# Optimization experiments

Hardware: AMD Instinct MI355X
Metric: run time of the kernel (lower is better)

Reference implementation:

```python
import jax, jax.numpy as jnp
import numpy as np

R, IN, H, O = 4, 1024, 4, 1024
HID4 = H * O  # 4096, GATConv output after flatten(1)
N_PRE, N_HYP, N_COMB = 1024, 1024, 2048
E_PRE, E_HYP, E_COMB = 8192, 8192, 16384


def setup_inputs() -> dict:
    key = jax.random.key(0)
    ks = jax.random.split(key, 24)
    w = lambda i, shape: jax.random.normal(ks[i], shape, dtype=jnp.float32) * 0.02
    return {
        'x_pre': jax.random.normal(ks[0], (N_PRE, IN), dtype=jnp.float32),
        'x_hyp': jax.random.normal(ks[1], (N_HYP, IN), dtype=jnp.float32),
        'x_comb': jax.random.normal(ks[2], (N_COMB, IN), dtype=jnp.float32),
        'src_pre': jax.random.randint(ks[3], (R, E_PRE), 0, N_PRE, dtype=jnp.int32),
        'dst_pre': jax.random.randint(ks[4], (R, E_PRE), 0, N_PRE, dtype=jnp.int32),
        'src_hyp': jax.random.randint(ks[5], (R, E_HYP), 0, N_HYP, dtype=jnp.int32),
        'dst_hyp': jax.random.randint(ks[6], (R, E_HYP), 0, N_HYP, dtype=jnp.int32),
        'src_comb': jax.random.randint(ks[7], (R, E_COMB), 0, N_COMB, dtype=jnp.int32),
        'dst_comb': jax.random.randint(ks[8], (R, E_COMB), 0, N_COMB, dtype=jnp.int32),
        'W1': w(9, (R, IN, HID4)),
        'al1': w(10, (R, H, O)),
        'ar1': w(11, (R, H, O)),
        'b1': w(12, (R, HID4)),
        'res1': w(13, (R, IN, HID4)),
        'W2': w(14, (R, HID4, HID4)),
        'al2': w(15, (R, H, O)),
        'ar2': w(16, (R, H, O)),
        'b2': w(17, (R, HID4)),
        'Wp': w(18, (3 * HID4, 3 * 1024)),
        'bp': w(19, (3 * 1024,)),
        'Wc1': w(20, (3 * 1024, 1024)),
        'bc1': w(21, (1024,)),
        'Wc2': w(22, (1024, 3)),
        'bc2': w(23, (3,)),
    }


def _gat_rel(x, src, dst, W, al, ar, b, res, N, identity_res):
    # DGL GATConv (eval mode, dropout off): shared fc, edge softmax, residual, bias
    feat = (x @ W).reshape(N, H, O)                       # [N,H,O]
    el = (feat * al[None]).sum(-1)                        # [N,H]
    er = (feat * ar[None]).sum(-1)                        # [N,H]
    e = jax.nn.leaky_relu(el[src] + er[dst], 0.2)         # [E,H]
    m = jax.ops.segment_max(e, dst, num_segments=N)
    m = jnp.where(jnp.isfinite(m), m, 0.0)                # zero-in-degree safe
    p = jnp.exp(e - m[dst])
    s = jax.ops.segment_sum(p, dst, num_segments=N)
    alpha = p / jnp.where(s[dst] > 0, s[dst], 1.0)        # [E,H]
    out = jax.ops.segment_sum(alpha[:, :, None] * feat[src], dst, num_segments=N)
    resval = x.reshape(N, H, O) if identity_res else (x @ res).reshape(N, H, O)
    return out + resval + b.reshape(1, H, O)


def _hetero_conv(x, src_r, dst_r, W_r, al_r, ar_r, b_r, res_r, N):
    # HeteroGraphConv(aggregate='mean') over R relations, scan to bound memory
    acc0 = jnp.zeros((N, H, O), dtype=x.dtype)
    if res_r is None:
        def body(acc, rel):
            src, dst, W, al, ar, b = rel
            return acc + _gat_rel(x, src, dst, W, al, ar, b, None, N, True), None
        acc, _ = jax.lax.scan(body, acc0, (src_r, dst_r, W_r, al_r, ar_r, b_r))
    else:
        def body(acc, rel):
            src, dst, W, al, ar, b, res = rel
            return acc + _gat_rel(x, src, dst, W, al, ar, b, res, N, False), None
        acc, _ = jax.lax.scan(body, acc0, (src_r, dst_r, W_r, al_r, ar_r, b_r, res_r))
    return acc / R


def _rgat(x, src, dst, W1, al1, ar1, b1, res1, W2, al2, ar2, b2, N):
    h = _hetero_conv(x, src, dst, W1, al1, ar1, b1, res1, N)
    h = jax.nn.elu(h.reshape(N, HID4))                    # flatten(1) + ELU
    h = _hetero_conv(h, src, dst, W2, al2, ar2, b2, None, N)
    return h.reshape(N, HID4)


def reference(x_pre, x_hyp, x_comb, src_pre, dst_pre, src_hyp, dst_hyp,
              src_comb, dst_comb, W1, al1, ar1, b1, res1, W2, al2, ar2, b2,
              Wp, bp, Wc1, bc1, Wc2, bc2):
    rp = _rgat(x_pre, src_pre, dst_pre, W1, al1, ar1, b1, res1, W2, al2, ar2, b2, N_PRE).mean(0, keepdims=True)
    rh = _rgat(x_hyp, src_hyp, dst_hyp, W1, al1, ar1, b1, res1, W2, al2, ar2, b2, N_HYP).mean(0, keepdims=True)
    rc = _rgat(x_comb, src_comb, dst_comb, W1, al1, ar1, b1, res1, W2, al2, ar2, b2, N_COMB).mean(0, keepdims=True)
    z = jnp.concatenate([rp, rh, rc], axis=1) @ Wp + bp   # graph_repr_proj
    hcls = jax.nn.relu(z @ Wc1 + bc1)                     # classifier MLP (dropout off)
    return hcls @ Wc2 + bc2                               # logits [1, n_classes]
```

## Files before the change

kernel.cpp:

```cpp
#include <hip/hip_runtime.h>
#include <math.h>

#define HID 4096
#define NMAX 2048
#define EMAX 16384
#define RREL 4
#define NTOT 4096

typedef unsigned short ushortT;
typedef __attribute__((ext_vector_type(8))) short short8;
typedef __attribute__((ext_vector_type(4))) float floatx4;

#define GLDS(gp, lp)                                                                        \
  __builtin_amdgcn_global_load_lds((const __attribute__((address_space(1))) unsigned*)(gp), \
                                   (__attribute__((address_space(3))) unsigned*)(lp), 16, 0, 0)

__device__ __forceinline__ ushortT f2b(float f) {
  unsigned u = __float_as_uint(f);
  u = u + 0x7fffu + ((u >> 16) & 1u);
  return (ushortT)(u >> 16);
}
__device__ __forceinline__ float b2f_lo(unsigned u) { return __uint_as_float(u << 16); }
__device__ __forceinline__ float b2f_hi(unsigned u) { return __uint_as_float(u & 0xffff0000u); }
__device__ __forceinline__ float b2f1(ushortT u) { return __uint_as_float((unsigned)u << 16); }

__global__ __launch_bounds__(256) void convt_k(const float* __restrict__ W,
                                               ushortT* __restrict__ Wt, int K) {
  int bn = blockIdx.x * 32;
  int bk = blockIdx.y * 32;
  int t = threadIdx.x;
  __shared__ ushortT tile[32][40];
  int kr = t >> 3;
  int nc = (t & 7) * 4;
  float4 v = *(const float4*)(W + (size_t)(bk + kr) * 4096 + bn + nc);
  tile[nc + 0][kr] = f2b(v.x);
  tile[nc + 1][kr] = f2b(v.y);
  tile[nc + 2][kr] = f2b(v.z);
  tile[nc + 3][kr] = f2b(v.w);
  __syncthreads();
  int n = t >> 3, j = (t & 7) * 4;
  uint2 u;
  u.x = (unsigned)tile[n][j] | ((unsigned)tile[n][j + 1] << 16);
  u.y = (unsigned)tile[n][j + 2] | ((unsigned)tile[n][j + 3] << 16);
  *(uint2*)(Wt + (size_t)(bn + n) * K + bk + j) = u;
}

__global__ __launch_bounds__(256) void convtsum_k(const float* __restrict__ W,
                                                  ushortT* __restrict__ Wt, int K) {
  int bn = blockIdx.x * 32;
  int bk = blockIdx.y * 32;
  int t = threadIdx.x;
  __shared__ ushortT tile[32][40];
  int kr = t >> 3;
  int nc = (t & 7) * 4;
  const size_t S = (size_t)1024 * HID;
  size_t base = (size_t)(bk + kr) * 4096 + bn + nc;
  float4 v0 = *(const float4*)(W + base);
  float4 v1 = *(const float4*)(W + base + S);
  float4 v2 = *(const float4*)(W + base + 2 * S);
  float4 v3 = *(const float4*)(W + base + 3 * S);
  tile[nc + 0][kr] = f2b(v0.x + v1.x + v2.x + v3.x);
  tile[nc + 1][kr] = f2b(v0.y + v1.y + v2.y + v3.y);
  tile[nc + 2][kr] = f2b(v0.z + v1.z + v2.z + v3.z);
  tile[nc + 3][kr] = f2b(v0.w + v1.w + v2.w + v3.w);
  __syncthreads();
  int n = t >> 3, j = (t & 7) * 4;
  uint2 u;
  u.x = (unsigned)tile[n][j] | ((unsigned)tile[n][j + 1] << 16);
  u.y = (unsigned)tile[n][j + 2] | ((unsigned)tile[n][j + 3] << 16);
  *(uint2*)(Wt + (size_t)(bn + n) * K + bk + j) = u;
}

__global__ void f2b_k(const float* __restrict__ in, ushortT* __restrict__ out, int n8) {
  int i = blockIdx.x * 256 + threadIdx.x;
  if (i >= n8) return;
  const float4* p = (const float4*)in;
  float4 a = p[2 * i], b = p[2 * i + 1];
  uint4 u;
  u.x = (unsigned)f2b(a.x) | ((unsigned)f2b(a.y) << 16);
  u.y = (unsigned)f2b(a.z) | ((unsigned)f2b(a.w) << 16);
  u.z = (unsigned)f2b(b.x) | ((unsigned)f2b(b.y) << 16);
  u.w = (unsigned)f2b(b.z) | ((unsigned)f2b(b.w) << 16);
  *(uint4*)(out + 8 * i) = u;
}

#define MIDB()                                         \
  __builtin_amdgcn_s_barrier();                        \
  asm volatile("s_waitcnt lgkmcnt(0)" ::: "memory");   \
  __builtin_amdgcn_sched_barrier(0);                   \
  __builtin_amdgcn_s_setprio(1)

#define RD_A(BASE, MH)                                                              \
  _Pragma("unroll") for (int f = 0; f < 4; f++)                                     \
      a[f] = *(const short8*)&lds[(BASE) + (wm * 128 + (MH)*64 + f * 16 + lrow) * 32 + kcol];
#define RD_B(BASE)                                                                  \
  _Pragma("unroll") for (int n = 0; n < 4; n++)                                     \
      b[n] = *(const short8*)&lds[(BASE) + 8192 + (wn * 64 + n * 16 + lrow) * 32 + kcol];
#define MFMA_H(MH)                                                                  \
  _Pragma("unroll") for (int f = 0; f < 4; f++)                                     \
  _Pragma("unroll") for (int n = 0; n < 4; n++)                                     \
      acc[(MH)*4 + f][n] =                                                          \
          __builtin_amdgcn_mfma_f32_16x16x32_bf16(a[f], b[n], acc[(MH)*4 + f][n], 0, 0, 0);
#define SA(BUF, H, KT) GLDS(Asrc + (size_t)((H)*128) * K + (KT)*32, lds + (BUF)*16384 + (H)*4096 + t * 8)
#define SB(BUF, H, KT) GLDS(Bsrc + (size_t)((H)*128) * K + (KT)*32, lds + (BUF)*16384 + 8192 + (H)*4096 + t * 8)

__global__ __launch_bounds__(512, 1) void gemm256(const ushortT* __restrict__ A,
                                                  const ushortT* __restrict__ Bt,
                                                  float* __restrict__ C,
                                                  ushortT* __restrict__ Cb,
                                                  int K, int mode) {
  __shared__ ushortT lds[32768];
  const int t = threadIdx.x;
  int bid = blockIdx.x;
  int swz = (bid & 7) * 32 + (bid >> 3);
  const int row0 = (swz >> 4) * 256;
  const int col0 = (swz & 15) * 256;

  const int rA = t >> 2;
  const int c8l = ((t & 3) ^ (((t >> 5) & 1) << 1)) * 8;
  const ushortT* Asrc = A + (size_t)(row0 + rA) * K + c8l;
  const ushortT* Bsrc = Bt + (size_t)(col0 + rA) * K + c8l;

  const int wave = t >> 6, lane = t & 63;
  const int wm = wave >> 2, wn = wave & 3;
  const int lrow = lane & 15, lkg = lane >> 4;
  const int kcol = (lkg * 8) ^ (((lane >> 3) & 1) << 4);

  floatx4 acc[8][4];
#pragma unroll
  for (int f = 0; f < 8; f++)
#pragma unroll
    for (int n = 0; n < 4; n++) acc[f][n] = (floatx4){0.f, 0.f, 0.f, 0.f};
  short8 a[4], b[4];

  const int nT = K >> 5;
  const int nIt = nT >> 1;

  SA(0, 0, 0); SA(0, 1, 0); SB(0, 0, 0); SB(0, 1, 0);
  SB(1, 0, 1); SB(1, 1, 1);
  asm volatile("s_waitcnt vmcnt(2)" ::: "memory");
  __builtin_amdgcn_s_barrier();
  __builtin_amdgcn_sched_barrier(0);

#pragma unroll 1
  for (int it = 0; it < nIt; it++) {
    const int k1 = 2 * it + 1, k2 = 2 * it + 2, k3 = 2 * it + 3;
    const bool s2 = (k2 < nT), s3 = (k3 < nT);
    RD_A(0, 0); RD_B(0);
    SA(1, 0, k1); SA(1, 1, k1);
    MIDB();
    MFMA_H(0);
    __builtin_amdgcn_s_setprio(0);
    __builtin_amdgcn_s_barrier();
    __builtin_amdgcn_sched_barrier(0);
    RD_A(0, 1);
    if (s2) { SB(0, 0, k2); SB(0, 1, k2); }
    MIDB();
    MFMA_H(1);
    __builtin_amdgcn_s_setprio(0);
    if (s2) asm volatile("s_waitcnt vmcnt(2)" ::: "memory");
    else    asm volatile("s_waitcnt vmcnt(0)" ::: "memory");
    __builtin_amdgcn_s_barrier();
    __builtin_amdgcn_sched_barrier(0);
    RD_A(16384, 0); RD_B(16384);
    if (s2) { SA(0, 0, k2); SA(0, 1, k2); }
    MIDB();
    MFMA_H(0);
    __builtin_amdgcn_s_setprio(0);
    __builtin_amdgcn_s_barrier();
    __builtin_amdgcn_sched_barrier(0);
    RD_A(16384, 1);
    if (s3) { SB(1, 0, k3); SB(1, 1, k3); }
    MIDB();
    MFMA_H(1);
    __builtin_amdgcn_s_setprio(0);
    if (s3) asm volatile("s_waitcnt vmcnt(2)" ::: "memory");
    else    asm volatile("s_waitcnt vmcnt(0)" ::: "memory");
    __builtin_amdgcn_s_barrier();
    __builtin_amdgcn_sched_barrier(0);
  }

#pragma unroll
  for (int fr = 0; fr < 8; fr++) {
    int row = row0 + wm * 128 + fr * 16 + lkg * 4;
#pragma unroll
    for (int n = 0; n < 4; n++) {
      int col = col0 + wn * 64 + n * 16 + lrow;
#pragma unroll
      for (int j = 0; j < 4; j++) {
        size_t idx = (size_t)(row + j) * HID + col;
        if (mode == 0) C[idx] = acc[fr][n][j];
        else Cb[idx] = f2b(acc[fr][n][j]);
      }
    }
  }
}

__global__ __launch_bounds__(256) void el_er_k(const ushortT* __restrict__ featb,
                                               const float* __restrict__ al,
                                               const float* __restrict__ ar,
                                               float* __restrict__ el,
                                               float* __restrict__ er) {
  int n = blockIdx.x, t = threadIdx.x;
  const unsigned* row = (const unsigned*)(featb + (size_t)n * HID);
  float pel[4] = {}, per_[4] = {};
#pragma unroll
  for (int j = 0; j < 8; j++) {
    unsigned u = row[j * 256 + t];
    int col = (j * 256 + t) * 2;
    const int h = j >> 1;
    pel[h] += b2f_lo(u) * al[col] + b2f_hi(u) * al[col + 1];
    per_[h] += b2f_lo(u) * ar[col] + b2f_hi(u) * ar[col + 1];
  }
  __shared__ float red[256][9];
#pragma unroll
  for (int h = 0; h < 4; h++) { red[t][h] = pel[h]; red[t][4 + h] = per_[h]; }
  __syncthreads();
  for (int s = 128; s > 0; s >>= 1) {
    if (t < s)
#pragma unroll
      for (int j = 0; j < 8; j++) red[t][j] += red[t + s][j];
    __syncthreads();
  }
  if (t < 4) { el[n * 4 + t] = red[0][t]; er[n * 4 + t] = red[0][4 + t]; }
}

__global__ void count_k(const int* __restrict__ dst, int* __restrict__ counts, int E) {
  int r = blockIdx.y;
  int i = blockIdx.x * blockDim.x + threadIdx.x;
  if (i < E) atomicAdd(&counts[r * NMAX + dst[(size_t)r * E + i]], 1);
}

__global__ __launch_bounds__(256) void scan_k(const int* __restrict__ counts,
                                              int* __restrict__ row_ptr, int N) {
  const int* cnt = counts + blockIdx.x * NMAX;
  int* rp = row_ptr + blockIdx.x * (NMAX + 1);
  __shared__ int sums[256];
  int t = threadIdx.x;
  int per = (N + 255) / 256;
  int local[8];
  int base = t * per;
  int s = 0;
  for (int i = 0; i < per; i++) {
    int idx = base + i;
    int v = (idx < N) ? cnt[idx] : 0;
    s += v;
    local[i] = s;
  }
  sums[t] = s;
  __syncthreads();
  for (int off = 1; off < 256; off <<= 1) {
    int v = (t >= off) ? sums[t - off] : 0;
    __syncthreads();
    sums[t] += v;
    __syncthreads();
  }
  int offset = (t > 0) ? sums[t - 1] : 0;
  for (int i = 0; i < per; i++) {
    int idx = base + i;
    if (idx < N) rp[idx + 1] = offset + local[i];
  }
  if (t == 0) rp[0] = 0;
}

__global__ void scatter_k(const int* __restrict__ dst, int* __restrict__ cnt,
                          const int* __restrict__ row_ptr, int* __restrict__ edge_ord,
                          int E) {
  int r = blockIdx.y;
  int i = blockIdx.x * blockDim.x + threadIdx.x;
  if (i < E) {
    int d = dst[(size_t)r * E + i];
    int off = atomicAdd(&cnt[r * NMAX + d], 1);
    edge_ord[(size_t)r * EMAX + row_ptr[r * (NMAX + 1) + d] + off] = i;
  }
}

__global__ void sm_k(const int* __restrict__ sp0, const int* __restrict__ sp1,
                     const int* __restrict__ sp2,
                     const int* __restrict__ row_ptr, const int* __restrict__ edge_ord,
                     const float* __restrict__ el, const float* __restrict__ er,
                     float* __restrict__ p, float* __restrict__ rinv, int r) {
  int i = blockIdx.x * 256 + threadIdx.x;
  int gnode = i >> 2, h = i & 3;
  int g = (gnode < 2048) ? (gnode >> 10) : 2;
  int goff = (g == 2) ? 2048 : (g << 10);
  int n = gnode - goff;
  const int* rp = row_ptr + (g * RREL + r) * (NMAX + 1);
  int start = rp[n], end = rp[n + 1];
  float rv = 0.f;
  if (end > start) {
    const int* eo = edge_ord + ((size_t)g * RREL + r) * EMAX;
    const int* srcg = (g == 0) ? sp0 : (g == 1) ? sp1 : sp2;
    float erv = er[gnode * 4 + h];
    float m = -3.4e38f;
    for (int c = start; c < end; c++) {
      float v = el[(goff + srcg[eo[c]]) * 4 + h] + erv;
      v = v > 0.f ? v : 0.2f * v;
      m = fmaxf(m, v);
    }
    float s = 0.f;
    float* pg = p + (size_t)g * EMAX * 4;
    for (int c = start; c < end; c++) {
      int eid = eo[c];
      float v = el[(goff + srcg[eid]) * 4 + h] + erv;
      v = v > 0.f ? v : 0.2f * v;
      float pv = expf(v - m);
      pg[eid * 4 + h] = pv;
      s += pv;
    }
    rv = 1.f / s;
  }
  rinv[gnode * 4 + h] = rv;
}

__global__ __launch_bounds__(256) void agg_k(const ushortT* __restrict__ featb,
                                             const float* __restrict__ p,
                                             const float* __restrict__ rinv,
                                             const int* __restrict__ row_ptr,
                                             const int* __restrict__ edge_ord,
                                             const int* __restrict__ sp0,
                                             const int* __restrict__ sp1,
                                             const int* __restrict__ sp2,
                                             float* __restrict__ acc, int r) {
  int gnode = blockIdx.x;
  int g = (gnode < 2048) ? (gnode >> 10) : 2;
  int goff = (g == 2) ? 2048 : (g << 10);
  int n = gnode - goff;
  const int* rp = row_ptr + (g * RREL + r) * (NMAX + 1);
  int start = rp[n], end = rp[n + 1];
  if (end == start) return;
  const int* eo = edge_ord + ((size_t)g * RREL + r) * EMAX;
  const int* srcg = (g == 0) ? sp0 : (g == 1) ? sp1 : sp2;
  const float* pg = p + (size_t)g * EMAX * 4;
  __shared__ int s_src[256];
  __shared__ float s_al[256][4];
  int t = threadIdx.x;
  float o0[8] = {}, o1[8] = {};
  for (int c = start; c < end; c += 256) {
    int m = min(256, end - c);
    if (t < m) {
      int eid = eo[c + t];
      s_src[t] = srcg[eid];
#pragma unroll
      for (int h = 0; h < 4; h++) s_al[t][h] = pg[eid * 4 + h];
    }
    __syncthreads();
    for (int i = 0; i < m; i++) {
      const unsigned* frow = (const unsigned*)(featb + (size_t)(goff + s_src[i]) * HID);
      float a0 = s_al[i][0], a1 = s_al[i][1], a2 = s_al[i][2], a3 = s_al[i][3];
#pragma unroll
      for (int j = 0; j < 8; j++) {
        unsigned u = frow[j * 256 + t];
        float av = (j < 2) ? a0 : (j < 4) ? a1 : (j < 6) ? a2 : a3;
        o0[j] += av * b2f_lo(u);
        o1[j] += av * b2f_hi(u);
      }
    }
    __syncthreads();
  }
  float rv[4];
#pragma unroll
  for (int h = 0; h < 4; h++) rv[h] = rinv[gnode * 4 + h];
#pragma unroll
  for (int j = 0; j < 8; j++) {
    float sc = rv[j >> 1];
    float2* pa = (float2*)(acc + (size_t)gnode * HID + (size_t)(j * 256 + t) * 2);
    float2 v = *pa;
    v.x += o0[j] * sc;
    v.y += o1[j] * sc;
    *pa = v;
  }
}

__global__ __launch_bounds__(256) void finalize1_k(const float* __restrict__ acc,
                                                   const float* __restrict__ b1,
                                                   ushortT* __restrict__ hb, int total) {
  int i = blockIdx.x * 256 + threadIdx.x;
  if (i >= total) return;
  int col = i & (HID - 1);
  float bs = b1[col] + b1[HID + col] + b1[2 * HID + col] + b1[3 * HID + col];
  float v = (acc[i] + bs) * 0.25f;
  v = v > 0.f ? v : (expf(v) - 1.f);
  hb[i] = f2b(v);
}

__global__ __launch_bounds__(256) void finalize2_mean_k(const float* __restrict__ acc,
                                                        const ushortT* __restrict__ hb,
                                                        const float* __restrict__ b2,
                                                        float* __restrict__ gm, int Nn,
                                                        float invN) {
  int col = blockIdx.x * 256 + threadIdx.x;
  int r0 = blockIdx.y * 32;
  int r1 = min(r0 + 32, Nn);
  float bs = 0.25f * (b2[col] + b2[HID + col] + b2[2 * HID + col] + b2[3 * HID + col]);
  float p = 0.f;
  for (int r = r0; r < r1; r++) {
    size_t i = (size_t)r * HID + col;
    p += acc[i] * 0.25f + b2f1(hb[i]) + bs;
  }
  atomicAdd(&gm[col], p * invN);
}

__global__ void initvec_k(float* __restrict__ out, const float* __restrict__ b, int n) {
  int i = blockIdx.x * blockDim.x + threadIdx.x;
  if (i < n) out[i] = b[i];
}

__global__ __launch_bounds__(256) void matvec_k(const float* __restrict__ v,
                                                const float* __restrict__ W,
                                                float* __restrict__ out, int K, int Nout,
                                                int kchunk) {
  int j = blockIdx.x * 256 + threadIdx.x;
  if (j >= Nout) return;
  int k0 = blockIdx.y * kchunk;
  int k1 = min(k0 + kchunk, K);
  float p = 0.f;
  for (int k = k0; k < k1; k++) p += v[k] * W[(size_t)k * Nout + j];
  atomicAdd(&out[j], p);
}

__global__ __launch_bounds__(256) void final_k(const float* __restrict__ hc,
                                               const float* __restrict__ Wc2,
                                               const float* __restrict__ bc2,
                                               float* __restrict__ out) {
  __shared__ float red[256];
  int t = threadIdx.x;
  for (int c = 0; c < 3; c++) {
    float p = 0.f;
    for (int k = t; k < 1024; k += 256) {
      float v = hc[k];
      v = v > 0.f ? v : 0.f;
      p += v * Wc2[k * 3 + c];
    }
    red[t] = p;
    __syncthreads();
    for (int s = 128; s > 0; s >>= 1) {
      if (t < s) red[t] += red[t + s];
      __syncthreads();
    }
    if (t == 0) out[c] = red[0] + bc2[c];
    __syncthreads();
  }
}

extern "C" void kernel_launch(void* const* d_in, const int* in_sizes, int n_in,
                              void* d_out, int out_size, void* d_ws, size_t ws_size,
                              hipStream_t stream) {
  const float* x_pre = (const float*)d_in[0];
  const float* x_hyp = (const float*)d_in[1];
  const float* x_comb = (const float*)d_in[2];
  const int* src_pre = (const int*)d_in[3];
  const int* dst_pre = (const int*)d_in[4];
  const int* src_hyp = (const int*)d_in[5];
  const int* dst_hyp = (const int*)d_in[6];
  const int* src_comb = (const int*)d_in[7];
  const int* dst_comb = (const int*)d_in[8];
  const float* W1 = (const float*)d_in[9];
  const float* al1 = (const float*)d_in[10];
  const float* ar1 = (const float*)d_in[11];
  const float* b1 = (const float*)d_in[12];
  const float* res1 = (const float*)d_in[13];
  const float* W2 = (const float*)d_in[14];
  const float* al2 = (const float*)d_in[15];
  const float* ar2 = (const float*)d_in[16];
  const float* b2 = (const float*)d_in[17];
  const float* Wp = (const float*)d_in[18];
  const float* bp = (const float*)d_in[19];
  const float* Wc1 = (const float*)d_in[20];
  const float* bc1 = (const float*)d_in[21];
  const float* Wc2 = (const float*)d_in[22];
  const float* bc2 = (const float*)d_in[23];
  float* out = (float*)d_out;

  char* w = (char*)d_ws;
  size_t off = 0;
  auto alloc = [&](size_t bytes) -> void* {
    void* p = w + off;
    off = (off + bytes + 255) & ~(size_t)255;
    return p;
  };
  float* acc = (float*)alloc((size_t)NTOT * HID * 4);
  ushortT* hb = (ushortT*)alloc((size_t)NTOT * HID * 2);
  ushortT* featb = (ushortT*)alloc((size_t)NTOT * HID * 2);
  ushortT* xb = (ushortT*)alloc((size_t)NTOT * 1024 * 2);
  ushortT* Wt = (ushortT*)alloc((size_t)HID * HID * 2);
  float* el = (float*)alloc(NTOT * 4 * 4);
  float* er = (float*)alloc(NTOT * 4 * 4);
  float* pbuf = (float*)alloc((size_t)3 * EMAX * 4 * 4);
  float* rinv = (float*)alloc(NTOT * 4 * 4);
  int* row_ptr = (int*)alloc(3 * RREL * (NMAX + 1) * 4);
  int* edge_ord = (int*)alloc((size_t)3 * RREL * EMAX * 4);
  int* counts = (int*)alloc(RREL * NMAX * 4);
  float* gm = (float*)alloc(3 * HID * 4);
  float* z = (float*)alloc(3072 * 4);
  float* hc = (float*)alloc(1024 * 4);

  hipMemsetAsync(gm, 0, 3 * HID * 4, stream);

  struct GDesc { const float* x; const int* src; const int* dst; int N; int E; int goff; };
  GDesc gs[3] = {{x_pre, src_pre, dst_pre, 1024, 8192, 0},
                 {x_hyp, src_hyp, dst_hyp, 1024, 8192, 1024},
                 {x_comb, src_comb, dst_comb, 2048, 16384, 2048}};

  for (int g = 0; g < 3; g++) {
    int N = gs[g].N, E = gs[g].E;
    int eb = E / 256;
    int* rpG = row_ptr + g * RREL * (NMAX + 1);
    int* eoG = edge_ord + (size_t)g * RREL * EMAX;
    hipMemsetAsync(counts, 0, RREL * NMAX * 4, stream);
    count_k<<<dim3(eb, RREL), 256, 0, stream>>>(gs[g].dst, counts, E);
    scan_k<<<RREL, 256, 0, stream>>>(counts, rpG, N);
    hipMemsetAsync(counts, 0, RREL * NMAX * 4, stream);
    scatter_k<<<dim3(eb, RREL), 256, 0, stream>>>(gs[g].dst, counts, rpG, eoG, E);
  }

  for (int g = 0; g < 3; g++)
    f2b_k<<<gs[g].N * 1024 / 8 / 256, 256, 0, stream>>>(gs[g].x,
                                                        xb + (size_t)gs[g].goff * 1024,
                                                        gs[g].N * 1024 / 8);

  for (int layer = 0; layer < 2; layer++) {
    int K = (layer == 0) ? 1024 : HID;
    const ushortT* Ab = (layer == 0) ? xb : hb;
    const float* Wl = (layer == 0) ? W1 : W2;
    const float* all = (layer == 0) ? al1 : al2;
    const float* arl = (layer == 0) ? ar1 : ar2;
    dim3 convGrid(HID / 32, K / 32);

    if (layer == 0) {
      convtsum_k<<<convGrid, 256, 0, stream>>>(res1, Wt, 1024);
      gemm256<<<256, 512, 0, stream>>>(xb, Wt, acc, (ushortT*)nullptr, 1024, 0);
    } else {
      hipMemsetAsync(acc, 0, (size_t)NTOT * HID * 4, stream);
    }

    for (int r = 0; r < RREL; r++) {
      convt_k<<<convGrid, 256, 0, stream>>>(Wl + (size_t)r * K * HID, Wt, K);
      gemm256<<<256, 512, 0, stream>>>(Ab, Wt, (float*)nullptr, featb, K, 2);
      el_er_k<<<NTOT, 256, 0, stream>>>(featb, all + r * HID, arl + r * HID, el, er);
      const int* sp0 = src_pre + (size_t)r * 8192;
      const int* sp1 = src_hyp + (size_t)r * 8192;
      const int* sp2 = src_comb + (size_t)r * 16384;
      sm_k<<<NTOT * 4 / 256, 256, 0, stream>>>(sp0, sp1, sp2, row_ptr, edge_ord, el, er,
                                               pbuf, rinv, r);
      agg_k<<<NTOT, 256, 0, stream>>>(featb, pbuf, rinv, row_ptr, edge_ord, sp0, sp1, sp2,
                                      acc, r);
    }

    if (layer == 0) {
      finalize1_k<<<(size_t)NTOT * HID / 256, 256, 0, stream>>>(acc, b1, hb, NTOT * HID);
    } else {
      for (int g = 0; g < 3; g++) {
        dim3 fg(HID / 256, (gs[g].N + 31) / 32);
        finalize2_mean_k<<<fg, 256, 0, stream>>>(acc + (size_t)gs[g].goff * HID,
                                                 hb + (size_t)gs[g].goff * HID, b2,
                                                 gm + g * HID, gs[g].N, 1.0f / gs[g].N);
      }
    }
  }

  initvec_k<<<12, 256, 0, stream>>>(z, bp, 3072);
  {
    dim3 mg(3072 / 256, 48);
    matvec_k<<<mg, 256, 0, stream>>>(gm, Wp, z, 12288, 3072, 256);
  }
  initvec_k<<<4, 256, 0, stream>>>(hc, bc1, 1024);
  {
    dim3 mg(1024 / 256, 24);
    matvec_k<<<mg, 256, 0, stream>>>(z, Wc1, hc, 3072, 1024, 128);
  }
  final_k<<<1, 256, 0, stream>>>(hc, Wc2, bc2, out);
}
```

Measured before the change: 2.182 ms.

## Batch all four relations into one wide GEMM and fused aggregation

Transposes all four relation weights into a single 16384-column matrix and runs one GEMM producing features for every relation at once, instead of four separate GEMMs. The el/er, softmax and aggregation kernels now cover all relations in a single launch each, and aggregation sums over the relations inside one kernel, so the accumulator is read and written once and the layer-2 memset is gone. The goal is fewer launches, less accumulator traffic, and better GPU fill from a larger GEMM grid. The cost is a 4x larger feature buffer and more workspace.

```diff
diff --git a/kernel.cpp b/kernel.cpp
--- a/kernel.cpp
+++ b/kernel.cpp
@@ -6,6 +6,7 @@
 #define EMAX 16384
 #define RREL 4
 #define NTOT 4096
+#define NCOL 16384
 
 typedef unsigned short ushortT;
 typedef __attribute__((ext_vector_type(8))) short short8;
@@ -108,13 +109,14 @@
                                                   const ushortT* __restrict__ Bt,
                                                   float* __restrict__ C,
                                                   ushortT* __restrict__ Cb,
-                                                  int K, int mode) {
+                                                  int K, int ldc, int nbx, int mode) {
   __shared__ ushortT lds[32768];
   const int t = threadIdx.x;
   int bid = blockIdx.x;
-  int swz = (bid & 7) * 32 + (bid >> 3);
-  const int row0 = (swz >> 4) * 256;
-  const int col0 = (swz & 15) * 256;
+  int cpx = (nbx << 4) >> 3;
+  int swz = (bid & 7) * cpx + (bid >> 3);
+  const int row0 = (swz / nbx) * 256;
+  const int col0 = (swz % nbx) * 256;
 
   const int rA = t >> 2;
   const int c8l = ((t & 3) ^ (((t >> 5) & 1) << 1)) * 8;
@@ -188,7 +190,7 @@
       int col = col0 + wn * 64 + n * 16 + lrow;
 #pragma unroll
       for (int j = 0; j < 4; j++) {
-        size_t idx = (size_t)(row + j) * HID + col;
+        size_t idx = (size_t)(row + j) * ldc + col;
         if (mode == 0) C[idx] = acc[fr][n][j];
         else Cb[idx] = f2b(acc[fr][n][j]);
       }
@@ -196,21 +198,23 @@
   }
 }
 
-__global__ __launch_bounds__(256) void el_er_k(const ushortT* __restrict__ featb,
+__global__ __launch_bounds__(256) void el_er_k(const ushortT* __restrict__ featb4,
                                                const float* __restrict__ al,
                                                const float* __restrict__ ar,
                                                float* __restrict__ el,
                                                float* __restrict__ er) {
-  int n = blockIdx.x, t = threadIdx.x;
-  const unsigned* row = (const unsigned*)(featb + (size_t)n * HID);
+  int n = blockIdx.x, r = blockIdx.y, t = threadIdx.x;
+  const unsigned* row = (const unsigned*)(featb4 + (size_t)n * NCOL + r * HID);
+  const float* alr = al + r * HID;
+  const float* arr = ar + r * HID;
   float pel[4] = {}, per_[4] = {};
 #pragma unroll
   for (int j = 0; j < 8; j++) {
     unsigned u = row[j * 256 + t];
     int col = (j * 256 + t) * 2;
     const int h = j >> 1;
-    pel[h] += b2f_lo(u) * al[col] + b2f_hi(u) * al[col + 1];
-    per_[h] += b2f_lo(u) * ar[col] + b2f_hi(u) * ar[col + 1];
+    pel[h] += b2f_lo(u) * alr[col] + b2f_hi(u) * alr[col + 1];
+    per_[h] += b2f_lo(u) * arr[col] + b2f_hi(u) * arr[col + 1];
   }
   __shared__ float red[256][9];
 #pragma unroll
@@ -222,7 +226,10 @@
       for (int j = 0; j < 8; j++) red[t][j] += red[t + s][j];
     __syncthreads();
   }
-  if (t < 4) { el[n * 4 + t] = red[0][t]; er[n * 4 + t] = red[0][4 + t]; }
+  if (t < 4) {
+    el[((size_t)r * NTOT + n) * 4 + t] = red[0][t];
+    er[((size_t)r * NTOT + n) * 4 + t] = red[0][4 + t];
+  }
 }
 
 __global__ void count_k(const int* __restrict__ dst, int* __restrict__ counts, int E) {
@@ -279,7 +286,8 @@
                      const int* __restrict__ sp2,
                      const int* __restrict__ row_ptr, const int* __restrict__ edge_ord,
                      const float* __restrict__ el, const float* __restrict__ er,
-                     float* __restrict__ p, float* __restrict__ rinv, int r) {
+                     float* __restrict__ p, float* __restrict__ rinv) {
+  int r = blockIdx.y;
   int i = blockIdx.x * 256 + threadIdx.x;
   int gnode = i >> 2, h = i & 3;
   int g = (gnode < 2048) ? (gnode >> 10) : 2;
@@ -290,19 +298,22 @@
   float rv = 0.f;
   if (end > start) {
     const int* eo = edge_ord + ((size_t)g * RREL + r) * EMAX;
-    const int* srcg = (g == 0) ? sp0 : (g == 1) ? sp1 : sp2;
-    float erv = er[gnode * 4 + h];
+    const int* srcg = (g == 0) ? sp0 + (size_t)r * 8192
+                    : (g == 1) ? sp1 + (size_t)r * 8192
+                               : sp2 + (size_t)r * 16384;
+    const float* elr = el + (size_t)r * NTOT * 4;
+    float erv = er[((size_t)r * NTOT + gnode) * 4 + h];
     float m = -3.4e38f;
     for (int c = start; c < end; c++) {
-      float v = el[(goff + srcg[eo[c]]) * 4 + h] + erv;
+      float v = elr[(goff + srcg[eo[c]]) * 4 + h] + erv;
       v = v > 0.f ? v : 0.2f * v;
       m = fmaxf(m, v);
     }
     float s = 0.f;
-    float* pg = p + (size_t)g * EMAX * 4;
+    float* pg = p + (size_t)(r * 3 + g) * EMAX * 4;
     for (int c = start; c < end; c++) {
       int eid = eo[c];
-      float v = el[(goff + srcg[eid]) * 4 + h] + erv;
+      float v = elr[(goff + srcg[eid]) * 4 + h] + erv;
       v = v > 0.f ? v : 0.2f * v;
       float pv = expf(v - m);
       pg[eid * 4 + h] = pv;
@@ -310,65 +321,77 @@
     }
     rv = 1.f / s;
   }
-  rinv[gnode * 4 + h] = rv;
-}
-
-__global__ __launch_bounds__(256) void agg_k(const ushortT* __restrict__ featb,
-                                             const float* __restrict__ p,
-                                             const float* __restrict__ rinv,
-                                             const int* __restrict__ row_ptr,
-                                             const int* __restrict__ edge_ord,
-                                             const int* __restrict__ sp0,
-                                             const int* __restrict__ sp1,
-                                             const int* __restrict__ sp2,
-                                             float* __restrict__ acc, int r) {
+  rinv[((size_t)r * NTOT + gnode) * 4 + h] = rv;
+}
+
+__global__ __launch_bounds__(256) void agg4_k(const ushortT* __restrict__ featb4,
+                                              const float* __restrict__ p,
+                                              const float* __restrict__ rinv,
+                                              const int* __restrict__ row_ptr,
+                                              const int* __restrict__ edge_ord,
+                                              const int* __restrict__ sp0,
+                                              const int* __restrict__ sp1,
+                                              const int* __restrict__ sp2,
+                                              float* __restrict__ acc, int accmode) {
   int gnode = blockIdx.x;
   int g = (gnode < 2048) ? (gnode >> 10) : 2;
   int goff = (g == 2) ? 2048 : (g << 10);
   int n = gnode - goff;
-  const int* rp = row_ptr + (g * RREL + r) * (NMAX + 1);
-  int start = rp[n], end = rp[n + 1];
-  if (end == start) return;
-  const int* eo = edge_ord + ((size_t)g * RREL + r) * EMAX;
-  const int* srcg = (g == 0) ? sp0 : (g == 1) ? sp1 : sp2;
-  const float* pg = p + (size_t)g * EMAX * 4;
   __shared__ int s_src[256];
   __shared__ float s_al[256][4];
   int t = threadIdx.x;
   float o0[8] = {}, o1[8] = {};
-  for (int c = start; c < end; c += 256) {
-    int m = min(256, end - c);
-    if (t < m) {
-      int eid = eo[c + t];
-      s_src[t] = srcg[eid];
-#pragma unroll
-      for (int h = 0; h < 4; h++) s_al[t][h] = pg[eid * 4 + h];
-    }
-    __syncthreads();
-    for (int i = 0; i < m; i++) {
-      const unsigned* frow = (const unsigned*)(featb + (size_t)(goff + s_src[i]) * HID);
-      float a0 = s_al[i][0], a1 = s_al[i][1], a2 = s_al[i][2], a3 = s_al[i][3];
-#pragma unroll
-      for (int j = 0; j < 8; j++) {
-        unsigned u = frow[j * 256 + t];
-        float av = (j < 2) ? a0 : (j < 4) ? a1 : (j < 6) ? a2 : a3;
-        o0[j] += av * b2f_lo(u);
-        o1[j] += av * b2f_hi(u);
+  for (int r = 0; r < RREL; r++) {
+    const int* rp = row_ptr + (g * RREL + r) * (NMAX + 1);
+    int start = rp[n], end = rp[n + 1];
+    if (end == start) continue;
+    const int* eo = edge_ord + ((size_t)g * RREL + r) * EMAX;
+    const int* srcg = (g == 0) ? sp0 + (size_t)r * 8192
+                    : (g == 1) ? sp1 + (size_t)r * 8192
+                               : sp2 + (size_t)r * 16384;
+    const float* pg = p + (size_t)(r * 3 + g) * EMAX * 4;
+    const float* rvp = rinv + ((size_t)r * NTOT + gnode) * 4;
+    float rv0 = rvp[0], rv1 = rvp[1], rv2 = rvp[2], rv3 = rvp[3];
+    const ushortT* fb = featb4 + (size_t)r * HID;
+    for (int c = start; c < end; c += 256) {
+      int m = min(256, end - c);
+      if (t < m) {
+        int eid = eo[c + t];
+        s_src[t] = srcg[eid];
+        s_al[t][0] = pg[eid * 4 + 0] * rv0;
+        s_al[t][1] = pg[eid * 4 + 1] * rv1;
+        s_al[t][2] = pg[eid * 4 + 2] * rv2;
+        s_al[t][3] = pg[eid * 4 + 3] * rv3;
       }
-    }
-    __syncthreads();
-  }
-  float rv[4];
-#pragma unroll
-  for (int h = 0; h < 4; h++) rv[h] = rinv[gnode * 4 + h];
+      __syncthreads();
+      for (int i = 0; i < m; i++) {
+        const unsigned* frow = (const unsigned*)(fb + (size_t)(goff + s_src[i]) * NCOL);
+        float a0 = s_al[i][0], a1 = s_al[i][1], a2 = s_al[i][2], a3 = s_al[i][3];
+#pragma unroll
+        for (int j = 0; j < 8; j++) {
+          unsigned u = frow[j * 256 + t];
+          float av = (j < 2) ? a0 : (j < 4) ? a1 : (j < 6) ? a2 : a3;
+          o0[j] += av * b2f_lo(u);
+          o1[j] += av * b2f_hi(u);
+        }
+      }
+      __syncthreads();
+    }
+  }
 #pragma unroll
   for (int j = 0; j < 8; j++) {
-    float sc = rv[j >> 1];
     float2* pa = (float2*)(acc + (size_t)gnode * HID + (size_t)(j * 256 + t) * 2);
-    float2 v = *pa;
-    v.x += o0[j] * sc;
-    v.y += o1[j] * sc;
-    *pa = v;
+    if (accmode) {
+      float2 v = *pa;
+      v.x += o0[j];
+      v.y += o1[j];
+      *pa = v;
+    } else {
+      float2 v;
+      v.x = o0[j];
+      v.y = o1[j];
+      *pa = v;
+    }
   }
 }
 
@@ -481,13 +504,13 @@
   };
   float* acc = (float*)alloc((size_t)NTOT * HID * 4);
   ushortT* hb = (ushortT*)alloc((size_t)NTOT * HID * 2);
-  ushortT* featb = (ushortT*)alloc((size_t)NTOT * HID * 2);
+  ushortT* featb4 = (ushortT*)alloc((size_t)NTOT * NCOL * 2);
   ushortT* xb = (ushortT*)alloc((size_t)NTOT * 1024 * 2);
-  ushortT* Wt = (ushortT*)alloc((size_t)HID * HID * 2);
-  float* el = (float*)alloc(NTOT * 4 * 4);
-  float* er = (float*)alloc(NTOT * 4 * 4);
-  float* pbuf = (float*)alloc((size_t)3 * EMAX * 4 * 4);
-  float* rinv = (float*)alloc(NTOT * 4 * 4);
+  ushortT* Wt = (ushortT*)alloc((size_t)NCOL * HID * 2);
+  float* el = (float*)alloc((size_t)RREL * NTOT * 4 * 4);
+  float* er = (float*)alloc((size_t)RREL * NTOT * 4 * 4);
+  float* pbuf = (float*)alloc((size_t)RREL * 3 * EMAX * 4 * 4);
+  float* rinv = (float*)alloc((size_t)RREL * NTOT * 4 * 4);
   int* row_ptr = (int*)alloc(3 * RREL * (NMAX + 1) * 4);
   int* edge_ord = (int*)alloc((size_t)3 * RREL * EMAX * 4);
   int* counts = (int*)alloc(RREL * NMAX * 4);
@@ -529,23 +552,20 @@
 
     if (layer == 0) {
       convtsum_k<<<convGrid, 256, 0, stream>>>(res1, Wt, 1024);
-      gemm256<<<256, 512, 0, stream>>>(xb, Wt, acc, (ushortT*)nullptr, 1024, 0);
-    } else {
-      hipMemsetAsync(acc, 0, (size_t)NTOT * HID * 4, stream);
-    }
-
-    for (int r = 0; r < RREL; r++) {
-      convt_k<<<convGrid, 256, 0, stream>>>(Wl + (size_t)r * K * HID, Wt, K);
-      gemm256<<<256, 512, 0, stream>>>(Ab, Wt, (float*)nullptr, featb, K, 2);
-      el_er_k<<<NTOT, 256, 0, stream>>>(featb, all + r * HID, arl + r * HID, el, er);
-      const int* sp0 = src_pre + (size_t)r * 8192;
-      const int* sp1 = src_hyp + (size_t)r * 8192;
-      const int* sp2 = src_comb + (size_t)r * 16384;
-      sm_k<<<NTOT * 4 / 256, 256, 0, stream>>>(sp0, sp1, sp2, row_ptr, edge_ord, el, er,
-                                               pbuf, rinv, r);
-      agg_k<<<NTOT, 256, 0, stream>>>(featb, pbuf, rinv, row_ptr, edge_ord, sp0, sp1, sp2,
-                                      acc, r);
-    }
+      gemm256<<<256, 512, 0, stream>>>(xb, Wt, acc, (ushortT*)nullptr, 1024, HID, 16, 0);
+    }
+
+    for (int r = 0; r < RREL; r++)
+      convt_k<<<convGrid, 256, 0, stream>>>(Wl + (size_t)r * K * HID,
+                                            Wt + (size_t)r * HID * K, K);
+    gemm256<<<1024, 512, 0, stream>>>(Ab, Wt, (float*)nullptr, featb4, K, NCOL, 64, 2);
+
+    el_er_k<<<dim3(NTOT, RREL), 256, 0, stream>>>(featb4, all, arl, el, er);
+    sm_k<<<dim3(NTOT * 4 / 256, RREL), 256, 0, stream>>>(src_pre, src_hyp, src_comb,
+                                                         row_ptr, edge_ord, el, er, pbuf,
+                                                         rinv);
+    agg4_k<<<NTOT, 256, 0, stream>>>(featb4, pbuf, rinv, row_ptr, edge_ord, src_pre,
+                                     src_hyp, src_comb, acc, layer == 0 ? 1 : 0);
 
     if (layer == 0) {
       finalize1_k<<<(size_t)NTOT * HID / 256, 256, 0, stream>>>(acc, b1, hb, NTOT * HID);
```

Result: faster. 2.014 ms (-7.7%).
